# Kernel optimization log

Hardware: AMD Instinct MI355X
Metric: run time of the kernel (lower is better)

The kernel has to match this reference:

```python
import jax, jax.numpy as jnp
import numpy as np

N_HEAD = 12
D_HEAD = 64


def setup_inputs() -> dict:
    key = jax.random.key(0)
    ks = jax.random.split(key, 9)
    bs, seq, d_model = 4, 2048, 768
    sc = 1.0 / np.sqrt(d_model)
    return {
        "q": jax.random.normal(ks[0], (bs, seq, d_model), jnp.float32),
        "k": jax.random.normal(ks[1], (bs, seq, d_model), jnp.float32),
        "v": jax.random.normal(ks[2], (bs, seq, d_model), jnp.float32),
        "Wq": jax.random.normal(ks[3], (d_model, d_model), jnp.float32) * sc,
        "bq": jax.random.normal(ks[4], (d_model,), jnp.float32) * 0.01,
        "Wk": jax.random.normal(ks[5], (d_model, d_model), jnp.float32) * sc,
        "bk": jax.random.normal(ks[6], (d_model,), jnp.float32) * 0.01,
        "Wv": jax.random.normal(ks[7], (d_model, d_model), jnp.float32) * sc,
        "bv": jax.random.normal(ks[8], (d_model,), jnp.float32) * 0.01,
    }


def _split_heads(x):
    # [bs, seq, n_head*d_head] -> [bs, n_head, seq, d_head]
    bs, seq, _ = x.shape
    return x.reshape(bs, seq, N_HEAD, D_HEAD).transpose(0, 2, 1, 3)


def reference(q, k, v, Wq, bq, Wk, bk, Wv, bv):
    # Linear projections (torch Linear: x @ W.T + b)
    wq = _split_heads(q @ Wq.T + bq)
    wk = _split_heads(k @ Wk.T + bk)
    wv = _split_heads(v @ Wv.T + bv)
    # scale=False in defaults -> raw dot products, no mask, dropout is eval no-op
    scores = jnp.einsum("bhqd,bhkd->bhqk", wq, wk)  # [bs, h, S, S]
    probs = jax.nn.softmax(scores, axis=-1)
    attn_vec = jnp.einsum("bhqk,bhkd->bhqd", probs, wv)
    bs, _, seq, _ = attn_vec.shape
    # merge heads -> [bs, seq, n_head*d_head]
    return attn_vec.transpose(0, 2, 1, 3).reshape(bs, seq, N_HEAD * D_HEAD)
```

## Files before the change

kernel.cpp:

```cpp
#include <hip/hip_runtime.h>
#include <stdint.h>

typedef _Float16 half8  __attribute__((ext_vector_type(8)));
typedef _Float16 half4v __attribute__((ext_vector_type(4)));
typedef float    floatx4 __attribute__((ext_vector_type(4)));

#define LOG2E 1.44269504088896340736f

__device__ __forceinline__ void gl_lds16(const _Float16* g, _Float16* l) {
  __builtin_amdgcn_global_load_lds(
      (__attribute__((address_space(1))) void*)g,
      (__attribute__((address_space(3))) void*)l, 16, 0, 0);
}

__device__ __forceinline__ half4v pack4(float a, float b, float c, float d) {
  auto lo = __builtin_amdgcn_cvt_pkrtz(a, b);
  auto hi = __builtin_amdgcn_cvt_pkrtz(c, d);
  return half4v{static_cast<_Float16>(lo[0]), static_cast<_Float16>(lo[1]),
                static_cast<_Float16>(hi[0]), static_cast<_Float16>(hi[1])};
}

struct CvtArgs {
  const float* src[6];
  _Float16*    dst[6];
  int          n[6];
};

__global__ void cvt_kernel(CvtArgs a) {
  const int z = blockIdx.y;
  const int n = a.n[z];
  const int i = (blockIdx.x * 256 + threadIdx.x) * 8;
  if (i >= n) return;
  const float4* s = (const float4*)(a.src[z] + i);
  float4 v0 = s[0], v1 = s[1];
  half8 h = { (_Float16)v0.x, (_Float16)v0.y, (_Float16)v0.z, (_Float16)v0.w,
              (_Float16)v1.x, (_Float16)v1.y, (_Float16)v1.z, (_Float16)v1.w };
  *(half8*)(a.dst[z] + i) = h;
}

__global__ __launch_bounds__(256, 2) void qkv_gemm(
    const _Float16* __restrict__ xh, const _Float16* __restrict__ wh,
    const float* __restrict__ bqp, const float* __restrict__ bkp, const float* __restrict__ bvp,
    _Float16* __restrict__ oq, _Float16* __restrict__ ok, _Float16* __restrict__ ovt)
{
  __shared__ __attribute__((aligned(16))) _Float16 As[128 * 32];
  __shared__ __attribute__((aligned(16))) _Float16 Bs[128 * 32];
  const int z  = blockIdx.z;
  const _Float16* X = xh + (size_t)z * 8192 * 768;
  const _Float16* W = wh + (size_t)z * 768 * 768;
  const int m0 = blockIdx.x * 128, n0 = blockIdx.y * 128;
  const int tid  = threadIdx.x;
  const int lane = tid & 63, wid = tid >> 6;
  const int wr = wid >> 1, wc = wid & 1;
  const int qd = lane >> 4, col = lane & 15;

  const floatx4 z4 = {0.f, 0.f, 0.f, 0.f};
  floatx4 acc[4][4];
  #pragma unroll
  for (int i = 0; i < 4; ++i)
    #pragma unroll
    for (int j = 0; j < 4; ++j) acc[i][j] = z4;

  const int c0 = tid, c1 = 256 + tid;
  const int ar0 = c0 >> 2, ac0 = (c0 & 3) * 8;
  const int ar1 = c1 >> 2, ac1 = (c1 & 3) * 8;

  for (int k0 = 0; k0 < 768; k0 += 32) {
    __syncthreads();
    gl_lds16(X + (size_t)(m0 + ar0) * 768 + k0 + ac0, As + c0 * 8);
    gl_lds16(X + (size_t)(m0 + ar1) * 768 + k0 + ac1, As + c1 * 8);
    gl_lds16(W + (size_t)(n0 + ar0) * 768 + k0 + ac0, Bs + c0 * 8);
    gl_lds16(W + (size_t)(n0 + ar1) * 768 + k0 + ac1, Bs + c1 * 8);
    __syncthreads();
    half8 af[4], bf[4];
    #pragma unroll
    for (int t = 0; t < 4; ++t)
      af[t] = *(const half8*)(As + (wr * 64 + t * 16 + col) * 32 + qd * 8);
    #pragma unroll
    for (int t = 0; t < 4; ++t)
      bf[t] = *(const half8*)(Bs + (wc * 64 + t * 16 + col) * 32 + qd * 8);
    if (z == 2) {
      #pragma unroll
      for (int i = 0; i < 4; ++i)
        #pragma unroll
        for (int j = 0; j < 4; ++j)
          acc[i][j] = __builtin_amdgcn_mfma_f32_16x16x32_f16(af[i], bf[j], acc[i][j], 0, 0, 0);
    } else {
      #pragma unroll
      for (int i = 0; i < 4; ++i)
        #pragma unroll
        for (int j = 0; j < 4; ++j)
          acc[i][j] = __builtin_amdgcn_mfma_f32_16x16x32_f16(bf[j], af[i], acc[i][j], 0, 0, 0);
    }
  }

  const float* bias = (z == 0) ? bqp : ((z == 1) ? bkp : bvp);
  if (z == 2) {
    #pragma unroll
    for (int j = 0; j < 4; ++j) {
      int n = n0 + wc * 64 + j * 16 + col;
      float bb = bias[n];
      #pragma unroll
      for (int i = 0; i < 4; ++i) {
        int m = m0 + wr * 64 + i * 16 + qd * 4;
        int b = m >> 11, s = m & 2047;
        half4v h;
        #pragma unroll
        for (int r = 0; r < 4; ++r) h[r] = (_Float16)(acc[i][j][r] + bb);
        *(half4v*)(ovt + ((size_t)(b * 768 + n)) * 2048 + s) = h;
      }
    }
  } else {
    _Float16* O = (z == 0) ? oq : ok;
    const float scale = (z == 0) ? LOG2E : 1.0f;
    #pragma unroll
    for (int j = 0; j < 4; ++j) {
      int n = n0 + wc * 64 + j * 16 + qd * 4;
      float4 bb = *(const float4*)(bias + n);
      int hh = n >> 6, d = n & 63;
      #pragma unroll
      for (int i = 0; i < 4; ++i) {
        int m = m0 + wr * 64 + i * 16 + col;
        int b = m >> 11, s = m & 2047;
        half4v h;
        h[0] = (_Float16)((acc[i][j][0] + bb.x) * scale);
        h[1] = (_Float16)((acc[i][j][1] + bb.y) * scale);
        h[2] = (_Float16)((acc[i][j][2] + bb.z) * scale);
        h[3] = (_Float16)((acc[i][j][3] + bb.w) * scale);
        *(half4v*)(O + (size_t)(b * 12 + hh) * 131072 + (size_t)s * 64 + d) = h;
      }
    }
  }
}


__device__ __forceinline__ void stage_kv(const _Float16* __restrict__ Kg,
                                         const _Float16* __restrict__ Vg,
                                         _Float16* ksd, _Float16* vsd, int j0, int tid) {
  #pragma unroll
  for (int i = 0; i < 2; ++i) {
    int c = i * 256 + tid;
    int row = c >> 3, sc = c & 7;
    gl_lds16(Kg + (size_t)(j0 + row) * 64 + ((sc ^ (row & 7)) * 8), ksd + c * 8);
    gl_lds16(Vg + (size_t)row * 2048 + j0 + ((sc ^ (row & 7)) * 8), vsd + c * 8);
  }
}

template <int BUF>
__device__ __forceinline__ void attn_body(
    int jnext, const _Float16* __restrict__ Kg, const _Float16* __restrict__ Vg,
    _Float16* Ks, _Float16* Vs, int tid,
    const half8 (&qf)[2][2], int kb0, int kb1, const int (&vb)[4],
    floatx4 (&negm)[2], floatx4 (&ol)[2], floatx4 (&o)[4][2])
{
  if (jnext < 2048)
    stage_kv(Kg, Vg, Ks + (1 - BUF) * 4096, Vs + (1 - BUF) * 4096, jnext, tid);

  const char* ksb = (const char*)Ks;
  const char* vsb = (const char*)Vs;

  floatx4 st[4][2];
  #pragma unroll
  for (int t = 0; t < 4; ++t) {
    half8 kf0 = *(const half8*)(ksb + BUF * 8192 + t * 2048 + kb0);
    half8 kf1 = *(const half8*)(ksb + BUF * 8192 + t * 2048 + kb1);
    #pragma unroll
    for (int qt = 0; qt < 2; ++qt) {
      st[t][qt] = __builtin_amdgcn_mfma_f32_16x16x32_f16(kf0, qf[qt][0], negm[qt], 0, 0, 0);
      st[t][qt] = __builtin_amdgcn_mfma_f32_16x16x32_f16(kf1, qf[qt][1], st[t][qt], 0, 0, 0);
    }
  }

  float mr[2];
  #pragma unroll
  for (int qt = 0; qt < 2; ++qt) {
    float v = fmaxf(
        fmaxf(fmaxf(fmaxf(st[0][qt][0], st[0][qt][1]), fmaxf(st[0][qt][2], st[0][qt][3])),
              fmaxf(fmaxf(st[1][qt][0], st[1][qt][1]), fmaxf(st[1][qt][2], st[1][qt][3]))),
        fmaxf(fmaxf(fmaxf(st[2][qt][0], st[2][qt][1]), fmaxf(st[2][qt][2], st[2][qt][3])),
              fmaxf(fmaxf(st[3][qt][0], st[3][qt][1]), fmaxf(st[3][qt][2], st[3][qt][3]))));
    v = fmaxf(v, __shfl_xor(v, 16, 64));
    v = fmaxf(v, __shfl_xor(v, 32, 64));
    mr[qt] = fmaxf(v, 0.f);
  }

  half4v pf[4][2];
  #pragma unroll
  for (int qt = 0; qt < 2; ++qt)
    #pragma unroll
    for (int t = 0; t < 4; ++t)
      pf[t][qt] = pack4(__builtin_amdgcn_exp2f(st[t][qt][0] - mr[qt]),
                        __builtin_amdgcn_exp2f(st[t][qt][1] - mr[qt]),
                        __builtin_amdgcn_exp2f(st[t][qt][2] - mr[qt]),
                        __builtin_amdgcn_exp2f(st[t][qt][3] - mr[qt]));

  if (__any(mr[0] > 0.f || mr[1] > 0.f)) {
    #pragma unroll
    for (int qt = 0; qt < 2; ++qt) {
      float al = __builtin_amdgcn_exp2f(-mr[qt]);
      negm[qt] -= mr[qt];
      ol[qt] *= al;
      #pragma unroll
      for (int dt = 0; dt < 4; ++dt) o[dt][qt] *= al;
    }
  }

  const half4v vone = {(_Float16)1.0f, (_Float16)1.0f, (_Float16)1.0f, (_Float16)1.0f};
  #pragma unroll
  for (int dt = 0; dt < 4; ++dt) {
    #pragma unroll
    for (int t = 0; t < 4; ++t) {
      half4v vf = *(const half4v*)(vsb + BUF * 8192 + dt * 2048 + vb[t]);
      #pragma unroll
      for (int qt = 0; qt < 2; ++qt)
        o[dt][qt] = __builtin_amdgcn_mfma_f32_16x16x16f16(vf, pf[t][qt], o[dt][qt], 0, 0, 0);
    }
  }
  #pragma unroll
  for (int t = 0; t < 4; ++t)
    #pragma unroll
    for (int qt = 0; qt < 2; ++qt)
      ol[qt] = __builtin_amdgcn_mfma_f32_16x16x16f16(vone, pf[t][qt], ol[qt], 0, 0, 0);

  __syncthreads();
}

__global__ __launch_bounds__(256, 3) void attn_kernel(
    const _Float16* __restrict__ Qm,
    const _Float16* __restrict__ Km,
    const _Float16* __restrict__ Vt,
    float* __restrict__ out)
{
  __shared__ __attribute__((aligned(16))) _Float16 Ks[2 * 4096];
  __shared__ __attribute__((aligned(16))) _Float16 Vs[2 * 4096];
  const int bh = blockIdx.y;
  const int q0 = blockIdx.x * 128;
  const int tid = threadIdx.x, lane = tid & 63, w = tid >> 6;
  const int qd = lane >> 4, col = lane & 15, c7 = col & 7;
  const _Float16* Qg = Qm + (size_t)bh * 131072;
  const _Float16* Kg = Km + (size_t)bh * 131072;
  const _Float16* Vg = Vt + (size_t)bh * 131072;

  half8 qf[2][2];
  #pragma unroll
  for (int qt = 0; qt < 2; ++qt)
    #pragma unroll
    for (int ks = 0; ks < 2; ++ks)
      qf[qt][ks] = *(const half8*)(Qg + (size_t)(q0 + w * 32 + qt * 16 + col) * 64
                                   + (ks * 4 + qd) * 8);

  const int kb0 = col * 128 + ((qd ^ c7) * 16);
  const int kb1 = col * 128 + (((4 + qd) ^ c7) * 16);
  const int vq = (qd >> 1) ^ c7;
  int vb[4];
  #pragma unroll
  for (int t = 0; t < 4; ++t)
    vb[t] = col * 128 + (qd & 1) * 8 + ((vq ^ (2 * t)) * 16);

  floatx4 negm[2] = {{100.f, 100.f, 100.f, 100.f}, {100.f, 100.f, 100.f, 100.f}};
  const floatx4 z4 = {0.f, 0.f, 0.f, 0.f};
  floatx4 ol[2] = {z4, z4};
  floatx4 o[4][2];
  #pragma unroll
  for (int dt = 0; dt < 4; ++dt)
    #pragma unroll
    for (int qt = 0; qt < 2; ++qt) o[dt][qt] = z4;

  stage_kv(Kg, Vg, Ks, Vs, 0, tid);
  __syncthreads();

  for (int jj = 0; jj < 2048; jj += 128) {
    attn_body<0>(jj + 64,  Kg, Vg, Ks, Vs, tid, qf, kb0, kb1, vb, negm, ol, o);
    attn_body<1>(jj + 128, Kg, Vg, Ks, Vs, tid, qf, kb0, kb1, vb, negm, ol, o);
  }

  const int b = bh / 12, h = bh % 12;
  #pragma unroll
  for (int qt = 0; qt < 2; ++qt) {
    float inv = 1.0f / ol[qt][0];
    int qg = q0 + w * 32 + qt * 16 + col;
    float* obase = out + ((size_t)b * 2048 + qg) * 768 + h * 64;
    #pragma unroll
    for (int dt = 0; dt < 4; ++dt) {
      floatx4 v = o[dt][qt];
      v *= inv;
      *(floatx4*)(obase + dt * 16 + qd * 4) = v;
    }
  }
}

extern "C" void kernel_launch(void* const* d_in, const int* in_sizes, int n_in,
                              void* d_out, int out_size, void* d_ws, size_t ws_size,
                              hipStream_t stream) {
  const float* q  = (const float*)d_in[0];
  const float* k  = (const float*)d_in[1];
  const float* v  = (const float*)d_in[2];
  const float* Wq = (const float*)d_in[3];
  const float* bq = (const float*)d_in[4];
  const float* Wk = (const float*)d_in[5];
  const float* bk = (const float*)d_in[6];
  const float* Wv = (const float*)d_in[7];
  const float* bv = (const float*)d_in[8];

  const size_t NX = 6291456;
  const size_t NW = 589824;
  const size_t need = (3 * NX + 3 * NW + 3 * NX) * sizeof(_Float16);
  if (ws_size < need) return;

  _Float16* xh = (_Float16*)d_ws;
  _Float16* wh = xh + 3 * NX;
  _Float16* qh = wh + 3 * NW;
  _Float16* kh = qh + NX;
  _Float16* vt = kh + NX;

  CvtArgs ca;
  ca.src[0] = q;  ca.src[1] = k;  ca.src[2] = v;
  ca.src[3] = Wq; ca.src[4] = Wk; ca.src[5] = Wv;
  ca.dst[0] = xh;          ca.dst[1] = xh + NX;     ca.dst[2] = xh + 2 * NX;
  ca.dst[3] = wh;          ca.dst[4] = wh + NW;     ca.dst[5] = wh + 2 * NW;
  ca.n[0] = (int)NX; ca.n[1] = (int)NX; ca.n[2] = (int)NX;
  ca.n[3] = (int)NW; ca.n[4] = (int)NW; ca.n[5] = (int)NW;

  cvt_kernel<<<dim3(3072, 6), 256, 0, stream>>>(ca);
  qkv_gemm<<<dim3(64, 6, 3), 256, 0, stream>>>(xh, wh, bq, bk, bv, qh, kh, vt);
  attn_kernel<<<dim3(16, 48), 256, 0, stream>>>(qh, kh, vt, (float*)d_out);
}
```

Before: 263.8 us.

## Fuse fp32 activation conversion into QKV GEMM with double-buffered swizzled LDS

Drops the separate fp16 conversion pass over the q/k/v activations. The GEMM now streams fp32 activations straight into LDS and converts them to fp16 while loading fragments; only the weights are still converted beforehand. It also double-buffers the LDS tiles with XOR swizzling, so the next tile loads while the current one computes and bank conflicts drop. This saves a full read and write of the activation tensors. In exchange the GEMM reads twice as many bytes for the A operand, uses twice the LDS, and does extra conversion work per tile, which may reduce occupancy.

Result: no change. 267.9 us (+1.5%).

```diff
diff --git a/kernel.cpp b/kernel.cpp
--- a/kernel.cpp
+++ b/kernel.cpp
@@ -8,6 +8,11 @@
 #define LOG2E 1.44269504088896340736f
 
 __device__ __forceinline__ void gl_lds16(const _Float16* g, _Float16* l) {
+  __builtin_amdgcn_global_load_lds(
+      (__attribute__((address_space(1))) void*)g,
+      (__attribute__((address_space(3))) void*)l, 16, 0, 0);
+}
+__device__ __forceinline__ void gl_lds16f(const float* g, float* l) {
   __builtin_amdgcn_global_load_lds(
       (__attribute__((address_space(1))) void*)g,
       (__attribute__((address_space(3))) void*)l, 16, 0, 0);
@@ -19,18 +24,20 @@
   return half4v{static_cast<_Float16>(lo[0]), static_cast<_Float16>(lo[1]),
                 static_cast<_Float16>(hi[0]), static_cast<_Float16>(hi[1])};
 }
+__device__ __forceinline__ half8 cvt8(floatx4 a, floatx4 b) {
+  half4v lo = pack4(a[0], a[1], a[2], a[3]);
+  half4v hi = pack4(b[0], b[1], b[2], b[3]);
+  return __builtin_shufflevector(lo, hi, 0, 1, 2, 3, 4, 5, 6, 7);
+}
 
 struct CvtArgs {
-  const float* src[6];
-  _Float16*    dst[6];
-  int          n[6];
+  const float* src[3];
+  _Float16*    dst[3];
 };
 
 __global__ void cvt_kernel(CvtArgs a) {
   const int z = blockIdx.y;
-  const int n = a.n[z];
   const int i = (blockIdx.x * 256 + threadIdx.x) * 8;
-  if (i >= n) return;
   const float4* s = (const float4*)(a.src[z] + i);
   float4 v0 = s[0], v1 = s[1];
   half8 h = { (_Float16)v0.x, (_Float16)v0.y, (_Float16)v0.z, (_Float16)v0.w,
@@ -38,16 +45,77 @@
   *(half8*)(a.dst[z] + i) = h;
 }
 
+
+__device__ __forceinline__ void gemm_stage(const float* __restrict__ X,
+                                           const _Float16* __restrict__ W,
+                                           float* Asb, _Float16* Bsb,
+                                           int m0, int n0, int k0, int tid) {
+  #pragma unroll
+  for (int i = 0; i < 4; ++i) {
+    int G = i * 256 + tid;
+    int r = G >> 3, gl = G & 7;
+    int g = gl ^ (r & 7);
+    gl_lds16f(X + (size_t)(m0 + r) * 768 + k0 + g * 4, Asb + G * 4);
+  }
+  #pragma unroll
+  for (int i = 0; i < 2; ++i) {
+    int G = i * 256 + tid;
+    int r = G >> 2, gl = G & 3;
+    int g = gl ^ ((r >> 1) & 3);
+    gl_lds16(W + (size_t)(n0 + r) * 768 + k0 + g * 8, Bsb + G * 8);
+  }
+}
+
+template <int BUF>
+__device__ __forceinline__ void gemm_body(
+    int knext, const float* __restrict__ X, const _Float16* __restrict__ W,
+    float* As, _Float16* Bs, int m0, int n0, int tid, int z,
+    int wr, int wc, int qd, int col, floatx4 (&acc)[4][4])
+{
+  if (knext < 768)
+    gemm_stage(X, W, As + (1 - BUF) * 4096, Bs + (1 - BUF) * 4096, m0, n0, knext, tid);
+
+  half8 af[4], bf[4];
+  #pragma unroll
+  for (int t = 0; t < 4; ++t) {
+    int ra = wr * 64 + t * 16 + col;
+    const float* Ab = As + BUF * 4096 + ra * 32;
+    floatx4 a0 = *(const floatx4*)(Ab + (((2 * qd)     ^ (ra & 7)) * 4));
+    floatx4 a1 = *(const floatx4*)(Ab + (((2 * qd + 1) ^ (ra & 7)) * 4));
+    af[t] = cvt8(a0, a1);
+  }
+  #pragma unroll
+  for (int t = 0; t < 4; ++t) {
+    int rb = wc * 64 + t * 16 + col;
+    bf[t] = *(const half8*)(Bs + BUF * 4096 + rb * 32 + ((qd ^ ((rb >> 1) & 3)) * 8));
+  }
+  if (z == 2) {
+    #pragma unroll
+    for (int i = 0; i < 4; ++i)
+      #pragma unroll
+      for (int j = 0; j < 4; ++j)
+        acc[i][j] = __builtin_amdgcn_mfma_f32_16x16x32_f16(af[i], bf[j], acc[i][j], 0, 0, 0);
+  } else {
+    #pragma unroll
+    for (int i = 0; i < 4; ++i)
+      #pragma unroll
+      for (int j = 0; j < 4; ++j)
+        acc[i][j] = __builtin_amdgcn_mfma_f32_16x16x32_f16(bf[j], af[i], acc[i][j], 0, 0, 0);
+  }
+  __syncthreads();
+}
+
 __global__ __launch_bounds__(256, 2) void qkv_gemm(
-    const _Float16* __restrict__ xh, const _Float16* __restrict__ wh,
+    const float* __restrict__ qx, const float* __restrict__ kx, const float* __restrict__ vx,
+    const _Float16* __restrict__ wh,
     const float* __restrict__ bqp, const float* __restrict__ bkp, const float* __restrict__ bvp,
     _Float16* __restrict__ oq, _Float16* __restrict__ ok, _Float16* __restrict__ ovt)
 {
-  __shared__ __attribute__((aligned(16))) _Float16 As[128 * 32];
-  __shared__ __attribute__((aligned(16))) _Float16 Bs[128 * 32];
+  __shared__ __attribute__((aligned(16))) float    As[2 * 4096];
+  __shared__ __attribute__((aligned(16))) _Float16 Bs[2 * 4096];
   const int z  = blockIdx.z;
-  const _Float16* X = xh + (size_t)z * 8192 * 768;
-  const _Float16* W = wh + (size_t)z * 768 * 768;
+  const float* X = (z == 0) ? qx : ((z == 1) ? kx : vx);
+  const _Float16* W = wh + (size_t)z * 589824;
   const int m0 = blockIdx.x * 128, n0 = blockIdx.y * 128;
   const int tid  = threadIdx.x;
   const int lane = tid & 63, wid = tid >> 6;
@@ -61,37 +129,11 @@
     #pragma unroll
     for (int j = 0; j < 4; ++j) acc[i][j] = z4;
 
-  const int c0 = tid, c1 = 256 + tid;
-  const int ar0 = c0 >> 2, ac0 = (c0 & 3) * 8;
-  const int ar1 = c1 >> 2, ac1 = (c1 & 3) * 8;
-
-  for (int k0 = 0; k0 < 768; k0 += 32) {
-    __syncthreads();
-    gl_lds16(X + (size_t)(m0 + ar0) * 768 + k0 + ac0, As + c0 * 8);
-    gl_lds16(X + (size_t)(m0 + ar1) * 768 + k0 + ac1, As + c1 * 8);
-    gl_lds16(W + (size_t)(n0 + ar0) * 768 + k0 + ac0, Bs + c0 * 8);
-    gl_lds16(W + (size_t)(n0 + ar1) * 768 + k0 + ac1, Bs + c1 * 8);
-    __syncthreads();
-    half8 af[4], bf[4];
-    #pragma unroll
-    for (int t = 0; t < 4; ++t)
-      af[t] = *(const half8*)(As + (wr * 64 + t * 16 + col) * 32 + qd * 8);
-    #pragma unroll
-    for (int t = 0; t < 4; ++t)
-      bf[t] = *(const half8*)(Bs + (wc * 64 + t * 16 + col) * 32 + qd * 8);
-    if (z == 2) {
-      #pragma unroll
-      for (int i = 0; i < 4; ++i)
-        #pragma unroll
-        for (int j = 0; j < 4; ++j)
-          acc[i][j] = __builtin_amdgcn_mfma_f32_16x16x32_f16(af[i], bf[j], acc[i][j], 0, 0, 0);
-    } else {
-      #pragma unroll
-      for (int i = 0; i < 4; ++i)
-        #pragma unroll
-        for (int j = 0; j < 4; ++j)
-          acc[i][j] = __builtin_amdgcn_mfma_f32_16x16x32_f16(bf[j], af[i], acc[i][j], 0, 0, 0);
-    }
+  gemm_stage(X, W, As, Bs, m0, n0, 0, tid);
+  __syncthreads();
+  for (int kk = 0; kk < 768; kk += 64) {
+    gemm_body<0>(kk + 32, X, W, As, Bs, m0, n0, tid, z, wr, wc, qd, col, acc);
+    gemm_body<1>(kk + 64, X, W, As, Bs, m0, n0, tid, z, wr, wc, qd, col, acc);
   }
 
   const float* bias = (z == 0) ? bqp : ((z == 1) ? bkp : bvp);
@@ -304,24 +346,19 @@
 
   const size_t NX = 6291456;
   const size_t NW = 589824;
-  const size_t need = (3 * NX + 3 * NW + 3 * NX) * sizeof(_Float16);
+  const size_t need = (3 * NW + 3 * NX) * sizeof(_Float16);
   if (ws_size < need) return;
 
-  _Float16* xh = (_Float16*)d_ws;
-  _Float16* wh = xh + 3 * NX;
+  _Float16* wh = (_Float16*)d_ws;
   _Float16* qh = wh + 3 * NW;
   _Float16* kh = qh + NX;
   _Float16* vt = kh + NX;
 
   CvtArgs ca;
-  ca.src[0] = q;  ca.src[1] = k;  ca.src[2] = v;
-  ca.src[3] = Wq; ca.src[4] = Wk; ca.src[5] = Wv;
-  ca.dst[0] = xh;          ca.dst[1] = xh + NX;     ca.dst[2] = xh + 2 * NX;
-  ca.dst[3] = wh;          ca.dst[4] = wh + NW;     ca.dst[5] = wh + 2 * NW;
-  ca.n[0] = (int)NX; ca.n[1] = (int)NX; ca.n[2] = (int)NX;
-  ca.n[3] = (int)NW; ca.n[4] = (int)NW; ca.n[5] = (int)NW;
-
-  cvt_kernel<<<dim3(3072, 6), 256, 0, stream>>>(ca);
-  qkv_gemm<<<dim3(64, 6, 3), 256, 0, stream>>>(xh, wh, bq, bk, bv, qh, kh, vt);
+  ca.src[0] = Wq; ca.src[1] = Wk; ca.src[2] = Wv;
+  ca.dst[0] = wh; ca.dst[1] = wh + NW; ca.dst[2] = wh + 2 * NW;
+
+  cvt_kernel<<<dim3(288, 3), 256, 0, stream>>>(ca);
+  qkv_gemm<<<dim3(64, 6, 3), 256, 0, stream>>>(q, k, v, wh, bq, bk, bv, qh, kh, vt);
   attn_kernel<<<dim3(16, 48), 256, 0, stream>>>(qh, kh, vt, (float*)d_out);
 }
```
